# Kernel tuning notes

Hardware: AMD Instinct MI355X
Metric: run time of the kernel (lower is better)

The kernel has to match this reference:

```python
import jax, jax.numpy as jnp
import numpy as np


def setup_inputs() -> dict:
    key = jax.random.key(0)
    B, C, H, W, A, G = 16, 512, 16, 16, 64, 256
    # Ragged group sizes (constant, deterministic) -> padded gather indices + mask
    rng = np.random.default_rng(0)
    sizes = rng.integers(32, 257, size=G)
    N = int(sizes.sum())          # ~36849 total sound tokens
    S_max = int(sizes.max())      # 256
    offsets = np.concatenate([[0], np.cumsum(sizes)[:-1]])
    pad_idx = np.zeros((G, S_max), dtype=np.int64)
    pad_mask = np.zeros((G, S_max), dtype=bool)
    for g in range(G):
        s = int(sizes[g])
        pad_idx[g, :s] = offsets[g] + np.arange(s)
        pad_mask[g, :s] = True
    k1, k2 = jax.random.split(key)
    return {
        'Z_img': jax.random.normal(k1, (B, C, H, W), jnp.float32),
        'Z_snd': jax.random.normal(k2, (N, C), jnp.float32),
        'pad_idx': jnp.asarray(pad_idx),
        'pad_mask': jnp.asarray(pad_mask),
        'attn_dims': A,
    }


def reference(Z_img, Z_snd, pad_idx, pad_mask, attn_dims):
    # Eval-mode forward of AudioAttention (no random subsampling).
    C = Z_img.shape[1]
    A = attn_dims
    # Global-average-pool image features: [B, C, H, W] -> [B, C]
    z = Z_img.reshape(Z_img.shape[0], C, -1).mean(axis=2)
    z_img, query = z[:, : C - A], z[:, C - A :]          # [B, C-A], [B, A]
    # Ragged groups as padded gather: [G, S, C]
    snd = Z_snd[pad_idx]
    value, key_ = snd[..., : C - A], snd[..., C - A :]   # [G,S,C-A], [G,S,A]
    # Per-group cross attention with the shared image queries
    scores = jnp.einsum('ba,gsa->gbs', query, key_)      # [G, B, S]
    scores = jnp.where(pad_mask[:, None, :], scores, -jnp.inf)
    attn = jax.nn.softmax(scores, axis=-1)               # padded cols -> 0 weight
    M_snd = jnp.einsum('gbs,gsc->gbc', attn, value)      # [G, B, C-A]
    M_img = jnp.broadcast_to(z_img[None], M_snd.shape)   # [G, B, C-A]
    return M_img, M_snd
```

## Files before the change

kernel.cpp:

```cpp
#include <hip/hip_runtime.h>
#include <math.h>

#define B_  16
#define C_  512
#define A_  64
#define CV  448
#define G_  256
#define HW  256
#define SMX 256
#define BSP 8

__global__ __launch_bounds__(256) void meanpool_kernel(const float* __restrict__ Zimg,
                                                       float* __restrict__ z) {
  int row  = (blockIdx.x << 2) + (threadIdx.x >> 6);
  int lane = threadIdx.x & 63;
  const float4* p = (const float4*)(Zimg + (size_t)row * HW);
  float4 v = p[lane];
  float s = (v.x + v.y) + (v.z + v.w);
  #pragma unroll
  for (int off = 32; off > 0; off >>= 1)
    s += __shfl_down(s, off, 64);
  if (lane == 0) z[row] = s * (1.0f / HW);
}

__global__ __launch_bounds__(256) void score_kernel(
    const float* __restrict__ Zsnd,
    const int*   __restrict__ pad_idx,
    const float* __restrict__ z,
    float*       __restrict__ attnW,
    int Smax, int N)
{
  const int bid  = blockIdx.x;
  const int g    = bid & 255;
  const int b0   = (bid >> 8) * BSP;
  const int t    = threadIdx.x;
  const int lane = t & 63;
  const int wave = t >> 6;

  __shared__ float qs[BSP * A_];
  __shared__ float red[4 * BSP];
  __shared__ float red2[4 * BSP];

  int myidx = -1;
  if (t < Smax) {
    int v = pad_idx[(size_t)g * Smax + t];
    bool ok = ((t == 0) || (v != 0)) && (v >= 0) && (v < N);
    myidx = ok ? v : -1;
  }
  const bool valid = (myidx >= 0);

  if (t < BSP * 16) {
    int b = t >> 4, a4 = t & 15;
    *(float4*)(qs + b * A_ + a4 * 4) =
        *(const float4*)(z + (b0 + b) * C_ + CV + a4 * 4);
  }
  __syncthreads();

  const float* krow = Zsnd + (size_t)(valid ? myidx : 0) * C_ + CV;
  float sc[BSP];
  #pragma unroll
  for (int b = 0; b < BSP; b++) sc[b] = 0.0f;

  #pragma unroll
  for (int c = 0; c < 4; c++) {
    float4 k0 = *(const float4*)(krow + c * 16 + 0);
    float4 k1 = *(const float4*)(krow + c * 16 + 4);
    float4 k2 = *(const float4*)(krow + c * 16 + 8);
    float4 k3 = *(const float4*)(krow + c * 16 + 12);
    #pragma unroll
    for (int b = 0; b < BSP; b++) {
      const float* qb = qs + b * A_ + c * 16;
      float4 q0 = *(const float4*)(qb + 0);
      float4 q1 = *(const float4*)(qb + 4);
      float4 q2 = *(const float4*)(qb + 8);
      float4 q3 = *(const float4*)(qb + 12);
      sc[b] += q0.x * k0.x + q0.y * k0.y + q0.z * k0.z + q0.w * k0.w
             + q1.x * k1.x + q1.y * k1.y + q1.z * k1.z + q1.w * k1.w
             + q2.x * k2.x + q2.y * k2.y + q2.z * k2.z + q2.w * k2.w
             + q3.x * k3.x + q3.y * k3.y + q3.z * k3.z + q3.w * k3.w;
    }
    __builtin_amdgcn_sched_barrier(0);
  }

  #pragma unroll
  for (int b = 0; b < BSP; b++) {
    float v = valid ? sc[b] : -INFINITY;
    #pragma unroll
    for (int off = 32; off > 0; off >>= 1)
      v = fmaxf(v, __shfl_xor(v, off, 64));
    if (lane == 0) red[wave * BSP + b] = v;
  }
  __syncthreads();

  float ex[BSP];
  #pragma unroll
  for (int b = 0; b < BSP; b++) {
    float gm = fmaxf(fmaxf(red[0 * BSP + b], red[1 * BSP + b]),
                     fmaxf(red[2 * BSP + b], red[3 * BSP + b]));
    float e = valid ? __expf(sc[b] - gm) : 0.0f;
    ex[b] = e;
    float es = e;
    #pragma unroll
    for (int off = 32; off > 0; off >>= 1)
      es += __shfl_xor(es, off, 64);
    if (lane == 0) red2[wave * BSP + b] = es;
  }
  __syncthreads();

  float* orow = attnW + ((size_t)g * SMX + t) * B_ + b0;
  float4 o0, o1;
  {
    float iv[BSP];
    #pragma unroll
    for (int b = 0; b < BSP; b++) {
      float gs = (red2[0 * BSP + b] + red2[1 * BSP + b]) +
                 (red2[2 * BSP + b] + red2[3 * BSP + b]);
      iv[b] = ex[b] / gs;
    }
    o0 = make_float4(iv[0], iv[1], iv[2], iv[3]);
    o1 = make_float4(iv[4], iv[5], iv[6], iv[7]);
  }
  *(float4*)(orow + 0) = o0;
  *(float4*)(orow + 4) = o1;
}

__global__ __launch_bounds__(256) void out_kernel(
    const float* __restrict__ Zsnd,
    const int*   __restrict__ pad_idx,
    const float* __restrict__ attnW,
    const float* __restrict__ z,
    float*       __restrict__ Mimg,
    float*       __restrict__ Msnd,
    int Smax, int N)
{
  const int bid  = blockIdx.x;
  const int g    = bid & 255;
  const int cs   = bid >> 8;
  const int c0   = cs * 128;
  const int w    = (cs == 3) ? 64 : 128;
  const int t    = threadIdx.x;
  const int lane = t & 63;
  const int wave = t >> 6;
  const int cl   = lane & 31;
  const int h    = lane >> 5;
  const int bh   = wave & 1;
  const int sh   = wave >> 1;
  const int b0   = bh * 8;

  __shared__ float attnT[SMX * B_];
  __shared__ int   idxs[SMX];
  __shared__ int   redi[4];

  int myidx = 0, sgv = 0;
  if (t < Smax) {
    int v = pad_idx[(size_t)g * Smax + t];
    bool ok = ((t == 0) || (v != 0)) && (v >= 0) && (v < N);
    myidx = ok ? v : 0;
    sgv   = ok ? (t + 1) : 0;
  }
  idxs[t] = myidx;
  #pragma unroll
  for (int off = 32; off > 0; off >>= 1)
    sgv = max(sgv, __shfl_xor(sgv, off, 64));
  if (lane == 0) redi[wave] = sgv;

  #pragma unroll
  for (int i = 0; i < 4; i++) {
    int li = i * 256 + t;
    *(float4*)(attnT + li * 4) = *(const float4*)(attnW + (size_t)g * (SMX * B_) + li * 4);
  }

  if (w == 128) {
    #pragma unroll
    for (int i = 0; i < 2; i++) {
      int li = i * 256 + t;
      int b = li >> 5, c4 = li & 31;
      *(float4*)(Mimg + (size_t)g * (B_ * CV) + b * CV + c0 + c4 * 4) =
          *(const float4*)(z + b * C_ + c0 + c4 * 4);
    }
  } else {
    int b = t >> 4, c4 = t & 15;
    *(float4*)(Mimg + (size_t)g * (B_ * CV) + b * CV + c0 + c4 * 4) =
        *(const float4*)(z + b * C_ + c0 + c4 * 4);
  }

  __syncthreads();
  const int sg   = max(max(redi[0], redi[1]), max(redi[2], redi[3]));
  const int sg32 = (sg + 31) & ~31;

  const float* vbase = Zsnd + c0 + cl * 4;
  float4 acc[8];
  #pragma unroll
  for (int b = 0; b < 8; b++) acc[b] = make_float4(0.f, 0.f, 0.f, 0.f);

  for (int s0 = 0; s0 < sg32; s0 += 32) {
    float4 v[8];
    int so[8];
    #pragma unroll
    for (int j = 0; j < 8; j++) {
      so[j] = s0 + 4 * j + 2 * sh + h;
      int idx = idxs[so[j]];
      v[j] = *(const float4*)(vbase + (size_t)idx * C_);
    }
    #pragma unroll
    for (int j = 0; j < 8; j++) {
      float4 w0 = *(const float4*)(attnT + so[j] * B_ + b0);
      float4 w1 = *(const float4*)(attnT + so[j] * B_ + b0 + 4);
      float4 vv = v[j];
      acc[0].x += w0.x * vv.x; acc[0].y += w0.x * vv.y; acc[0].z += w0.x * vv.z; acc[0].w += w0.x * vv.w;
      acc[1].x += w0.y * vv.x; acc[1].y += w0.y * vv.y; acc[1].z += w0.y * vv.z; acc[1].w += w0.y * vv.w;
      acc[2].x += w0.z * vv.x; acc[2].y += w0.z * vv.y; acc[2].z += w0.z * vv.z; acc[2].w += w0.z * vv.w;
      acc[3].x += w0.w * vv.x; acc[3].y += w0.w * vv.y; acc[3].z += w0.w * vv.z; acc[3].w += w0.w * vv.w;
      acc[4].x += w1.x * vv.x; acc[4].y += w1.x * vv.y; acc[4].z += w1.x * vv.z; acc[4].w += w1.x * vv.w;
      acc[5].x += w1.y * vv.x; acc[5].y += w1.y * vv.y; acc[5].z += w1.y * vv.z; acc[5].w += w1.y * vv.w;
      acc[6].x += w1.z * vv.x; acc[6].y += w1.z * vv.y; acc[6].z += w1.z * vv.z; acc[6].w += w1.z * vv.w;
      acc[7].x += w1.w * vv.x; acc[7].y += w1.w * vv.y; acc[7].z += w1.w * vv.z; acc[7].w += w1.w * vv.w;
    }
  }

  __syncthreads();
  float* redS = attnT;
  if (sh == 1) {
    #pragma unroll
    for (int b = 0; b < 8; b++)
      *(float4*)(redS + (((size_t)bh * 8 + b) * 64 + lane) * 4) = acc[b];
  }
  __syncthreads();
  if (sh == 0) {
    #pragma unroll
    for (int b = 0; b < 8; b++) {
      float4 o = *(const float4*)(redS + (((size_t)bh * 8 + b) * 64 + lane) * 4);
      acc[b].x += o.x; acc[b].y += o.y; acc[b].z += o.z; acc[b].w += o.w;
      acc[b].x += __shfl_xor(acc[b].x, 32, 64);
      acc[b].y += __shfl_xor(acc[b].y, 32, 64);
      acc[b].z += __shfl_xor(acc[b].z, 32, 64);
      acc[b].w += __shfl_xor(acc[b].w, 32, 64);
    }
    if (h == 0 && cl * 4 < w) {
      float* obase = Msnd + (size_t)g * (B_ * CV) + (size_t)b0 * CV + c0 + cl * 4;
      #pragma unroll
      for (int b = 0; b < 8; b++)
        *(float4*)(obase + b * CV) = acc[b];
    }
  }
}

extern "C" void kernel_launch(void* const* d_in, const int* in_sizes, int n_in,
                              void* d_out, int out_size, void* d_ws, size_t ws_size,
                              hipStream_t stream) {
  const float* Zimg   = (const float*)d_in[0];
  const float* Zsnd   = (const float*)d_in[1];
  const int*   padidx = (const int*)d_in[2];

  const int N    = in_sizes[1] / C_;
  const int Smax = in_sizes[2] / G_;

  float* z     = (float*)d_ws;
  float* attnW = z + B_ * C_;
  float* Mimg  = (float*)d_out;
  float* Msnd  = Mimg + (size_t)G_ * B_ * CV;

  meanpool_kernel<<<(B_ * C_) / 4, 256, 0, stream>>>(Zimg, z);
  score_kernel<<<G_ * 2, 256, 0, stream>>>(Zsnd, padidx, z, attnW, Smax, N);
  out_kernel<<<G_ * 4, 256, 0, stream>>>(Zsnd, padidx, attnW, z, Mimg, Msnd, Smax, N);
}
```

Baseline: 159.7 us.

## Fuse score/softmax and weighted-value kernels into one per-group kernel

Merges the score+softmax kernel and the attention-weighted value kernel into a single 512-thread kernel per (group, batch-half). Attention weights stay in shared memory instead of round-tripping through a global workspace, and one launch is removed. The key dot product is split across two threads per token, and the value pass now covers all channels per block rather than splitting channels across blocks. The trade-off is fewer blocks (512 vs 1024) for the value pass, and each value row is now read by both batch-half blocks of a group.

Result: faster. 154.5 us (-3.3%).

```diff
diff --git a/kernel.cpp b/kernel.cpp
--- a/kernel.cpp
+++ b/kernel.cpp
@@ -23,53 +23,80 @@
   if (lane == 0) z[row] = s * (1.0f / HW);
 }
 
-__global__ __launch_bounds__(256) void score_kernel(
+__global__ __launch_bounds__(512, 4) void fused_kernel(
     const float* __restrict__ Zsnd,
     const int*   __restrict__ pad_idx,
     const float* __restrict__ z,
-    float*       __restrict__ attnW,
+    float*       __restrict__ Mimg,
+    float*       __restrict__ Msnd,
     int Smax, int N)
 {
   const int bid  = blockIdx.x;
   const int g    = bid & 255;
-  const int b0   = (bid >> 8) * BSP;
+  const int bh   = bid >> 8;
+  const int b0   = bh * BSP;
   const int t    = threadIdx.x;
   const int lane = t & 63;
   const int wave = t >> 6;
 
   __shared__ float qs[BSP * A_];
-  __shared__ float red[4 * BSP];
-  __shared__ float red2[4 * BSP];
-
-  int myidx = -1;
-  if (t < Smax) {
+  __shared__ float attnT[SMX * BSP];
+  __shared__ int   idxs[SMX];
+  __shared__ float red[8 * BSP];
+  __shared__ float red2[8 * BSP];
+  __shared__ int   redi[8];
+  __shared__ float redS[4 * BSP * 64 * 4];
+
+  int sgv = 0;
+  if (t < SMX) {
     int v = pad_idx[(size_t)g * Smax + t];
     bool ok = ((t == 0) || (v != 0)) && (v >= 0) && (v < N);
-    myidx = ok ? v : -1;
-  }
-  const bool valid = (myidx >= 0);
+    idxs[t] = ok ? v : 0;
+    sgv = ok ? (t + 1) : 0;
+  }
+  #pragma unroll
+  for (int off = 32; off > 0; off >>= 1)
+    sgv = max(sgv, __shfl_xor(sgv, off, 64));
+  if (lane == 0) redi[wave] = sgv;
 
   if (t < BSP * 16) {
     int b = t >> 4, a4 = t & 15;
     *(float4*)(qs + b * A_ + a4 * 4) =
         *(const float4*)(z + (b0 + b) * C_ + CV + a4 * 4);
   }
-  __syncthreads();
-
-  const float* krow = Zsnd + (size_t)(valid ? myidx : 0) * C_ + CV;
+
+  {
+    int b = t >> 6, c = t & 63;
+    float* mrow = Mimg + (size_t)g * (B_ * CV) + (b0 + b) * CV;
+    const float* zrow = z + (b0 + b) * C_;
+    *(float4*)(mrow + c * 4) = *(const float4*)(zrow + c * 4);
+    int c2 = c + 64;
+    if (c2 < 112)
+      *(float4*)(mrow + c2 * 4) = *(const float4*)(zrow + c2 * 4);
+  }
+
+  __syncthreads();
+  const int sg = max(max(max(redi[0], redi[1]), max(redi[2], redi[3])),
+                     max(max(redi[4], redi[5]), max(redi[6], redi[7])));
+
+  const int s_ = t >> 1;
+  const int kh = t & 1;
+  const bool valid = (s_ < sg);
+  const float* krow = Zsnd + (size_t)idxs[s_] * C_ + CV + kh * 32;
+
   float sc[BSP];
   #pragma unroll
   for (int b = 0; b < BSP; b++) sc[b] = 0.0f;
 
   #pragma unroll
-  for (int c = 0; c < 4; c++) {
+  for (int c = 0; c < 2; c++) {
     float4 k0 = *(const float4*)(krow + c * 16 + 0);
     float4 k1 = *(const float4*)(krow + c * 16 + 4);
     float4 k2 = *(const float4*)(krow + c * 16 + 8);
     float4 k3 = *(const float4*)(krow + c * 16 + 12);
     #pragma unroll
     for (int b = 0; b < BSP; b++) {
-      const float* qb = qs + b * A_ + c * 16;
+      const float* qb = qs + b * A_ + kh * 32 + c * 16;
       float4 q0 = *(const float4*)(qb + 0);
       float4 q1 = *(const float4*)(qb + 4);
       float4 q2 = *(const float4*)(qb + 8);
@@ -81,6 +108,9 @@
     }
     __builtin_amdgcn_sched_barrier(0);
   }
+  #pragma unroll
+  for (int b = 0; b < BSP; b++)
+    sc[b] += __shfl_xor(sc[b], 1, 64);
 
   #pragma unroll
   for (int b = 0; b < BSP; b++) {
@@ -95,11 +125,12 @@
   float ex[BSP];
   #pragma unroll
   for (int b = 0; b < BSP; b++) {
-    float gm = fmaxf(fmaxf(red[0 * BSP + b], red[1 * BSP + b]),
-                     fmaxf(red[2 * BSP + b], red[3 * BSP + b]));
+    float gm = red[0 * BSP + b];
+    #pragma unroll
+    for (int w2 = 1; w2 < 8; w2++) gm = fmaxf(gm, red[w2 * BSP + b]);
     float e = valid ? __expf(sc[b] - gm) : 0.0f;
     ex[b] = e;
-    float es = e;
+    float es = (kh == 0) ? e : 0.0f;
     #pragma unroll
     for (int off = 32; off > 0; off >>= 1)
       es += __shfl_xor(es, off, 64);
@@ -107,105 +138,44 @@
   }
   __syncthreads();
 
-  float* orow = attnW + ((size_t)g * SMX + t) * B_ + b0;
-  float4 o0, o1;
-  {
+  if (kh == 0) {
     float iv[BSP];
     #pragma unroll
     for (int b = 0; b < BSP; b++) {
-      float gs = (red2[0 * BSP + b] + red2[1 * BSP + b]) +
-                 (red2[2 * BSP + b] + red2[3 * BSP + b]);
+      float gs = red2[0 * BSP + b];
+      #pragma unroll
+      for (int w2 = 1; w2 < 8; w2++) gs += red2[w2 * BSP + b];
       iv[b] = ex[b] / gs;
     }
-    o0 = make_float4(iv[0], iv[1], iv[2], iv[3]);
-    o1 = make_float4(iv[4], iv[5], iv[6], iv[7]);
-  }
-  *(float4*)(orow + 0) = o0;
-  *(float4*)(orow + 4) = o1;
-}
-
-__global__ __launch_bounds__(256) void out_kernel(
-    const float* __restrict__ Zsnd,
-    const int*   __restrict__ pad_idx,
-    const float* __restrict__ attnW,
-    const float* __restrict__ z,
-    float*       __restrict__ Mimg,
-    float*       __restrict__ Msnd,
-    int Smax, int N)
-{
-  const int bid  = blockIdx.x;
-  const int g    = bid & 255;
-  const int cs   = bid >> 8;
-  const int c0   = cs * 128;
-  const int w    = (cs == 3) ? 64 : 128;
-  const int t    = threadIdx.x;
-  const int lane = t & 63;
-  const int wave = t >> 6;
-  const int cl   = lane & 31;
-  const int h    = lane >> 5;
-  const int bh   = wave & 1;
-  const int sh   = wave >> 1;
-  const int b0   = bh * 8;
-
-  __shared__ float attnT[SMX * B_];
-  __shared__ int   idxs[SMX];
-  __shared__ int   redi[4];
-
-  int myidx = 0, sgv = 0;
-  if (t < Smax) {
-    int v = pad_idx[(size_t)g * Smax + t];
-    bool ok = ((t == 0) || (v != 0)) && (v >= 0) && (v < N);
-    myidx = ok ? v : 0;
-    sgv   = ok ? (t + 1) : 0;
-  }
-  idxs[t] = myidx;
-  #pragma unroll
-  for (int off = 32; off > 0; off >>= 1)
-    sgv = max(sgv, __shfl_xor(sgv, off, 64));
-  if (lane == 0) redi[wave] = sgv;
-
-  #pragma unroll
-  for (int i = 0; i < 4; i++) {
-    int li = i * 256 + t;
-    *(float4*)(attnT + li * 4) = *(const float4*)(attnW + (size_t)g * (SMX * B_) + li * 4);
-  }
-
-  if (w == 128) {
-    #pragma unroll
-    for (int i = 0; i < 2; i++) {
-      int li = i * 256 + t;
-      int b = li >> 5, c4 = li & 31;
-      *(float4*)(Mimg + (size_t)g * (B_ * CV) + b * CV + c0 + c4 * 4) =
-          *(const float4*)(z + b * C_ + c0 + c4 * 4);
-    }
-  } else {
-    int b = t >> 4, c4 = t & 15;
-    *(float4*)(Mimg + (size_t)g * (B_ * CV) + b * CV + c0 + c4 * 4) =
-        *(const float4*)(z + b * C_ + c0 + c4 * 4);
-  }
-
-  __syncthreads();
-  const int sg   = max(max(redi[0], redi[1]), max(redi[2], redi[3]));
+    *(float4*)(attnT + s_ * BSP + 0) = make_float4(iv[0], iv[1], iv[2], iv[3]);
+    *(float4*)(attnT + s_ * BSP + 4) = make_float4(iv[4], iv[5], iv[6], iv[7]);
+  }
+  __syncthreads();
+
+  const int ch = wave >> 1;
+  const int sh = wave & 1;
+  const int cl = lane & 31;
+  const int h  = lane >> 5;
+  const int c0 = ch * 128;
   const int sg32 = (sg + 31) & ~31;
 
   const float* vbase = Zsnd + c0 + cl * 4;
-  float4 acc[8];
-  #pragma unroll
-  for (int b = 0; b < 8; b++) acc[b] = make_float4(0.f, 0.f, 0.f, 0.f);
+  float4 acc[BSP];
+  #pragma unroll
+  for (int b = 0; b < BSP; b++) acc[b] = make_float4(0.f, 0.f, 0.f, 0.f);
 
   for (int s0 = 0; s0 < sg32; s0 += 32) {
     float4 v[8];
-    int so[8];
     #pragma unroll
     for (int j = 0; j < 8; j++) {
-      so[j] = s0 + 4 * j + 2 * sh + h;
-      int idx = idxs[so[j]];
-      v[j] = *(const float4*)(vbase + (size_t)idx * C_);
+      int so = s0 + 4 * j + 2 * sh + h;
+      v[j] = *(const float4*)(vbase + (size_t)idxs[so] * C_);
     }
     #pragma unroll
     for (int j = 0; j < 8; j++) {
-      float4 w0 = *(const float4*)(attnT + so[j] * B_ + b0);
-      float4 w1 = *(const float4*)(attnT + so[j] * B_ + b0 + 4);
+      int so = s0 + 4 * j + 2 * sh + h;
+      float4 w0 = *(const float4*)(attnT + so * BSP + 0);
+      float4 w1 = *(const float4*)(attnT + so * BSP + 4);
       float4 vv = v[j];
       acc[0].x += w0.x * vv.x; acc[0].y += w0.x * vv.y; acc[0].z += w0.x * vv.z; acc[0].w += w0.x * vv.w;
       acc[1].x += w0.y * vv.x; acc[1].y += w0.y * vv.y; acc[1].z += w0.y * vv.z; acc[1].w += w0.y * vv.w;
@@ -218,28 +188,26 @@
     }
   }
 
-  __syncthreads();
-  float* redS = attnT;
   if (sh == 1) {
     #pragma unroll
-    for (int b = 0; b < 8; b++)
-      *(float4*)(redS + (((size_t)bh * 8 + b) * 64 + lane) * 4) = acc[b];
+    for (int b = 0; b < BSP; b++)
+      *(float4*)(redS + (((size_t)ch * BSP + b) * 64 + lane) * 4) = acc[b];
   }
   __syncthreads();
   if (sh == 0) {
     #pragma unroll
-    for (int b = 0; b < 8; b++) {
-      float4 o = *(const float4*)(redS + (((size_t)bh * 8 + b) * 64 + lane) * 4);
+    for (int b = 0; b < BSP; b++) {
+      float4 o = *(const float4*)(redS + (((size_t)ch * BSP + b) * 64 + lane) * 4);
       acc[b].x += o.x; acc[b].y += o.y; acc[b].z += o.z; acc[b].w += o.w;
       acc[b].x += __shfl_xor(acc[b].x, 32, 64);
       acc[b].y += __shfl_xor(acc[b].y, 32, 64);
       acc[b].z += __shfl_xor(acc[b].z, 32, 64);
       acc[b].w += __shfl_xor(acc[b].w, 32, 64);
     }
-    if (h == 0 && cl * 4 < w) {
+    if (h == 0 && c0 + cl * 4 < CV) {
       float* obase = Msnd + (size_t)g * (B_ * CV) + (size_t)b0 * CV + c0 + cl * 4;
       #pragma unroll
-      for (int b = 0; b < 8; b++)
+      for (int b = 0; b < BSP; b++)
         *(float4*)(obase + b * CV) = acc[b];
     }
   }
@@ -255,12 +223,10 @@
   const int N    = in_sizes[1] / C_;
   const int Smax = in_sizes[2] / G_;
 
-  float* z     = (float*)d_ws;
-  float* attnW = z + B_ * C_;
-  float* Mimg  = (float*)d_out;
-  float* Msnd  = Mimg + (size_t)G_ * B_ * CV;
+  float* z    = (float*)d_ws;
+  float* Mimg = (float*)d_out;
+  float* Msnd = Mimg + (size_t)G_ * B_ * CV;
 
   meanpool_kernel<<<(B_ * C_) / 4, 256, 0, stream>>>(Zimg, z);
-  score_kernel<<<G_ * 2, 256, 0, stream>>>(Zsnd, padidx, z, attnW, Smax, N);
-  out_kernel<<<G_ * 4, 256, 0, stream>>>(Zsnd, padidx, attnW, z, Mimg, Msnd, Smax, N);
+  fused_kernel<<<G_ * 2, 512, 0, stream>>>(Zsnd, padidx, z, Mimg, Msnd, Smax, N);
 }
```
